# Optimization experiments

Measured on AMD Instinct MI355X. Metric: run time of the kernel, lower is better.

Reference implementation:

```python
import jax, jax.numpy as jnp
import numpy as np

N_NODES = 100000
N_EDGES = 1000000
D = 64
NUM_LAYERS = 2
NUM_REL = 3
BN_EPS = 1e-5


def setup_inputs() -> dict:
    key = jax.random.key(0)
    ks = jax.random.split(key, 10)
    h = jax.random.normal(ks[0], (N_NODES, D), dtype=jnp.float32)
    norm = jax.random.uniform(ks[1], (N_EDGES,), dtype=jnp.float32)
    src = jax.random.randint(ks[2], (N_EDGES,), 0, N_NODES, dtype=jnp.int32)
    dst = jax.random.randint(ks[3], (N_EDGES,), 0, N_NODES, dtype=jnp.int32)
    rel_type = jax.random.randint(ks[4], (N_EDGES,), 0, NUM_REL, dtype=jnp.int32)
    # learned params
    bound = np.sqrt(6.0 / D)  # kaiming_uniform fan_in, relu gain sqrt(2): sqrt(6/fan_in)
    weight = jax.random.uniform(ks[5], (NUM_REL, D, D), minval=-bound, maxval=bound, dtype=jnp.float32)
    s = 1.0 / np.sqrt(D)
    w_ih = jax.random.uniform(ks[6], (3 * D, D), minval=-s, maxval=s, dtype=jnp.float32)
    w_hh = jax.random.uniform(ks[7], (3 * D, D), minval=-s, maxval=s, dtype=jnp.float32)
    b_ih = jax.random.uniform(ks[8], (3 * D,), minval=-s, maxval=s, dtype=jnp.float32)
    b_hh = jax.random.uniform(ks[9], (3 * D,), minval=-s, maxval=s, dtype=jnp.float32)
    gamma = jnp.ones((D,), dtype=jnp.float32)
    beta = jnp.zeros((D,), dtype=jnp.float32)
    return {"h": h, "norm": norm, "weight": weight, "w_ih": w_ih, "w_hh": w_hh,
            "b_ih": b_ih, "b_hh": b_hh, "gamma": gamma, "beta": beta,
            "src": src, "dst": dst, "rel_type": rel_type}


def _gru_cell(x, h, w_ih, w_hh, b_ih, b_hh):
    # torch nn.GRU single-step math
    gi = x @ w_ih.T + b_ih  # [N, 3D]
    gh = h @ w_hh.T + b_hh
    i_r, i_z, i_n = jnp.split(gi, 3, axis=-1)
    h_r, h_z, h_n = jnp.split(gh, 3, axis=-1)
    r = jax.nn.sigmoid(i_r + h_r)
    z = jax.nn.sigmoid(i_z + h_z)
    n = jnp.tanh(i_n + r * h_n)
    return (1.0 - z) * n + z * h


def reference(h, norm, weight, w_ih, w_hh, b_ih, b_hh, gamma, beta, src, dst, rel_type):
    output = h
    hstate = jnp.zeros_like(h)
    for _ in range(NUM_LAYERS):
        # transform all node features by each relation weight, then gather per edge
        t = jnp.einsum('nd,rde->rne', output, weight)        # [R, N, D]
        msg = t[rel_type, src] * norm[:, None]               # [E, D]
        swh = jax.ops.segment_sum(msg, dst, num_segments=N_NODES)  # scatter-sum to dst
        hstate = _gru_cell(swh, hstate, w_ih, w_hh, b_ih, b_hh)
        output = hstate  # seq_len==1 GRU: output == new hidden state
    # BatchNorm1d (training mode, biased variance)
    mean = jnp.mean(output, axis=0)
    var = jnp.mean(jnp.square(output - mean), axis=0)
    return (output - mean) / jnp.sqrt(var + BN_EPS) * gamma + beta
```

## Files before the change

kernel.cpp:

```cpp
#include <hip/hip_runtime.h>

typedef __bf16 bf16x8 __attribute__((ext_vector_type(8)));
typedef float f32x4 __attribute__((ext_vector_type(4)));
typedef short short8 __attribute__((ext_vector_type(8)));

#define MFMA16(a, b, c) __builtin_amdgcn_mfma_f32_16x16x32_bf16(a, b, c, 0, 0, 0)

__device__ inline unsigned short bf16_rne(float x) {
  unsigned u = __builtin_bit_cast(unsigned, x);
  return (unsigned short)((u + 0x7FFFu + ((u >> 16) & 1u)) >> 16);
}
__device__ inline float bf16_tof(unsigned short s) {
  unsigned u = ((unsigned)s) << 16;
  return __builtin_bit_cast(float, u);
}
__device__ inline void split2(float x, unsigned short* hi, unsigned short* lo) {
  unsigned short h = bf16_rne(x);
  *hi = h;
  *lo = bf16_rne(x - bf16_tof(h));
}
__device__ inline float fast_rcp(float x) { return __builtin_amdgcn_rcpf(x); }


__global__ __launch_bounds__(256) void wprep_kernel(
    const float* __restrict__ W, const float* __restrict__ w_ih,
    const float* __restrict__ w_hh, unsigned short* __restrict__ frags) {
  int idx = blockIdx.x * 256 + threadIdx.x;
  if (idx < 1536) {
    int lane = idx & 63;
    int ks = (idx >> 6) % 6;
    int tci = idx / (6 * 64);
    int c = tci * 16 + (lane & 15);
    size_t dbase = ((size_t)(tci * 6 + ks) * 64 + lane) * 8;
#pragma unroll
    for (int j = 0; j < 8; ++j) {
      int k = ks * 32 + ((lane >> 4) << 3) + j;
      int r = k >> 6, d = k & 63;
      float v = W[(r << 12) + (d << 6) + c];
      unsigned short h, l;
      split2(v, &h, &l);
      frags[dbase + j] = h;
      frags[12288 + dbase + j] = l;
    }
  } else if (idx < 1536 + 2 * 1536) {
    int i2 = idx - 1536;
    int set = i2 / 1536;
    int i3 = i2 % 1536;
    int lane = i3 & 63;
    int ks = (i3 >> 6) & 1;
    int tci = (i3 >> 7) % 12;
    int c = tci * 16 + (lane & 15);
    unsigned short* hi = frags + (size_t)(2 + 2 * set) * 12288;
    unsigned short* lo = hi + 12288;
    size_t dbase = ((size_t)(tci * 2 + ks) * 64 + lane) * 8;
    const float* wsrc = set ? w_hh : w_ih;
#pragma unroll
    for (int j = 0; j < 8; ++j) {
      int k = ks * 32 + ((lane >> 4) << 3) + j;
      float v = wsrc[(c << 6) + k];
      unsigned short h, l;
      split2(v, &h, &l);
      hi[dbase + j] = h;
      lo[dbase + j] = l;
    }
  }
}


__global__ __launch_bounds__(256) void count_kernel(
    const int* __restrict__ dst, unsigned* __restrict__ counts, int E) {
  int base = (blockIdx.x * 256 + threadIdx.x) * 4;
  if (base + 4 <= E) {
    int4 d = *(const int4*)(dst + base);
    atomicAdd(&counts[d.x], 1u);
    atomicAdd(&counts[d.y], 1u);
    atomicAdd(&counts[d.z], 1u);
    atomicAdd(&counts[d.w], 1u);
  } else {
    for (int k = base; k < E; ++k) atomicAdd(&counts[dst[k]], 1u);
  }
}

__global__ __launch_bounds__(1024) void scan_k1(
    const unsigned* __restrict__ counts, unsigned* __restrict__ offs,
    unsigned* __restrict__ bsums, int N) {
  __shared__ unsigned sm[1024];
  int tid = threadIdx.x;
  int i = blockIdx.x * 1024 + tid;
  unsigned v = (i < N) ? counts[i] : 0u;
  sm[tid] = v;
  __syncthreads();
  for (int ofs = 1; ofs < 1024; ofs <<= 1) {
    unsigned add = (tid >= ofs) ? sm[tid - ofs] : 0u;
    __syncthreads();
    sm[tid] += add;
    __syncthreads();
  }
  if (i < N) offs[i] = sm[tid] - v;
  if (tid == 0) bsums[blockIdx.x] = sm[1023];
}

__global__ __launch_bounds__(128) void scan_k2(
    unsigned* __restrict__ bsums, unsigned* __restrict__ offs, int M, int N) {
  __shared__ unsigned sm[128];
  int tid = threadIdx.x;
  unsigned v = (tid < M) ? bsums[tid] : 0u;
  sm[tid] = v;
  __syncthreads();
  for (int ofs = 1; ofs < 128; ofs <<= 1) {
    unsigned add = (tid >= ofs) ? sm[tid - ofs] : 0u;
    __syncthreads();
    sm[tid] += add;
    __syncthreads();
  }
  if (tid < M) bsums[tid] = sm[tid] - v;
  if (tid == 127) offs[N] = sm[127];
}

__global__ __launch_bounds__(256) void scan_k3(
    unsigned* __restrict__ offs, const unsigned* __restrict__ bsums, int N) {
  int i = blockIdx.x * 256 + threadIdx.x;
  if (i < N) offs[i] = offs[i] + bsums[i >> 10];
}

__global__ __launch_bounds__(128) void bin_init_kernel(
    const unsigned* __restrict__ offs, unsigned* __restrict__ bincur, int nbins) {
  int b = threadIdx.x;
  if (b < nbins) bincur[b] = offs[b << 10];
}

#define SCHUNK 2048
__global__ __launch_bounds__(256) void bin_scatter_kernel(
    const int* __restrict__ src, const int* __restrict__ dst,
    const int* __restrict__ rel, const float* __restrict__ norm,
    unsigned* __restrict__ bincur, uint2* __restrict__ binbuf, int E) {
  __shared__ unsigned cnt[128];
  __shared__ unsigned base[128];
  int tid = threadIdx.x;
  int start = blockIdx.x * SCHUNK;
  if (tid < 128) cnt[tid] = 0u;
  __syncthreads();
  unsigned mybin[8];
  uint2 myrec[8];
#pragma unroll
  for (int i = 0; i < 8; ++i) {
    int e = start + i * 256 + tid;
    if (e < E) {
      int d = dst[e];
      mybin[i] = (unsigned)d >> 10;
      myrec[i].x = (unsigned)src[e] | ((unsigned)rel[e] << 17) |
                   ((unsigned)(d & 1023) << 19);
      myrec[i].y = __builtin_bit_cast(unsigned, norm[e]);
      atomicAdd(&cnt[mybin[i]], 1u);
    } else {
      mybin[i] = 0xFFFFFFFFu;
    }
  }
  __syncthreads();
  if (tid < 128) {
    unsigned c = cnt[tid];
    base[tid] = c ? atomicAdd(&bincur[tid], c) : 0u;
    cnt[tid] = 0u;
  }
  __syncthreads();
#pragma unroll
  for (int i = 0; i < 8; ++i) {
    if (mybin[i] != 0xFFFFFFFFu) {
      unsigned r = atomicAdd(&cnt[mybin[i]], 1u);
      binbuf[base[mybin[i]] + r] = myrec[i];
    }
  }
}

__global__ __launch_bounds__(1024) void bin_sort_kernel(
    const uint2* __restrict__ binbuf, const unsigned* __restrict__ offs,
    uint2* __restrict__ epack, unsigned* __restrict__ rcnt, int N) {
  __shared__ unsigned cnt[3 * 1024];
  __shared__ unsigned offl[1024];
  int bin = blockIdx.x;
  int base = bin << 10;
  int tid = threadIdx.x;
  int hi = base + 1024;
  if (hi > N) hi = N;
  if (base + tid < N) offl[tid] = offs[base + tid];
  cnt[tid] = 0u;
  cnt[1024 + tid] = 0u;
  cnt[2048 + tid] = 0u;
  __syncthreads();
  unsigned start = offs[base];
  unsigned end = offs[hi];
  for (unsigned j = start + tid; j < end; j += 1024) {
    uint2 rec = binbuf[j];
    unsigned dlo = rec.x >> 19;
    unsigned r = (rec.x >> 17) & 3;
    atomicAdd(&cnt[r * 1024 + dlo], 1u);
  }
  __syncthreads();
  unsigned c0 = cnt[tid], c1 = cnt[1024 + tid];
  int n = base + tid;
  if (n < N) rcnt[n] = c0 | (c1 << 16);
  unsigned o = (n < N) ? offl[tid] : 0u;
  cnt[tid] = o;
  cnt[1024 + tid] = o + c0;
  cnt[2048 + tid] = o + c0 + c1;
  __syncthreads();
  for (unsigned j = start + tid; j < end; j += 1024) {
    uint2 rec = binbuf[j];
    unsigned dlo = rec.x >> 19;
    unsigned r = (rec.x >> 17) & 3;
    unsigned p = atomicAdd(&cnt[r * 1024 + dlo], 1u);
    epack[p] = rec;
  }
}


template <int LAYER>
__global__ __launch_bounds__(256) void layer_kernel(
    const float* __restrict__ xf, const unsigned* __restrict__ offs,
    const unsigned* __restrict__ rcnt, const uint2* __restrict__ epack,
    const unsigned short* __restrict__ wft,
    const unsigned short* __restrict__ wfi, const unsigned short* __restrict__ wfh,
    const float* __restrict__ b_ih, const float* __restrict__ b_hh,
    float* __restrict__ outf, int N) {
  __shared__ float zld[16][197];
  __shared__ float swht[16][69];
  int tid = threadIdx.x;
  int n0 = blockIdx.x << 4;

  {
    int g = tid >> 4, l16 = tid & 15;
    int n = n0 + g;
    int c4 = l16 << 2;
    float z0[4] = {}, z1[4] = {}, z2[4] = {};
    if (n < N) {
      unsigned a = offs[n], b = offs[n + 1];
      unsigned rc = rcnt[n];
      unsigned b1 = a + (rc & 0xFFFFu), b2 = b1 + (rc >> 16);
      auto run = [&](unsigned s, unsigned e, float* z) {
        unsigned j = s;
        for (; j + 2 <= e; j += 2) {
          uint2 e0 = epack[j], e1 = epack[j + 1];
          float4 v0 = *(const float4*)(xf + (((size_t)(e0.x & 0x1FFFFu)) << 6) + c4);
          float4 v1 = *(const float4*)(xf + (((size_t)(e1.x & 0x1FFFFu)) << 6) + c4);
          float nv0 = __builtin_bit_cast(float, e0.y);
          float nv1 = __builtin_bit_cast(float, e1.y);
          z[0] = fmaf(nv0, v0.x, fmaf(nv1, v1.x, z[0]));
          z[1] = fmaf(nv0, v0.y, fmaf(nv1, v1.y, z[1]));
          z[2] = fmaf(nv0, v0.z, fmaf(nv1, v1.z, z[2]));
          z[3] = fmaf(nv0, v0.w, fmaf(nv1, v1.w, z[3]));
        }
        if (j < e) {
          uint2 e0 = epack[j];
          float4 v0 = *(const float4*)(xf + (((size_t)(e0.x & 0x1FFFFu)) << 6) + c4);
          float nv0 = __builtin_bit_cast(float, e0.y);
          z[0] = fmaf(nv0, v0.x, z[0]);
          z[1] = fmaf(nv0, v0.y, z[1]);
          z[2] = fmaf(nv0, v0.z, z[2]);
          z[3] = fmaf(nv0, v0.w, z[3]);
        }
      };
      run(a, b1, z0);
      run(b1, b2, z1);
      run(b2, b, z2);
    }
#pragma unroll
    for (int i = 0; i < 4; ++i) {
      zld[g][c4 + i] = z0[i];
      zld[g][64 + c4 + i] = z1[i];
      zld[g][128 + c4 + i] = z2[i];
    }
  }
  __syncthreads();

  int lane = tid & 63, w = tid >> 6;
  int r15 = lane & 15, kq = lane >> 4;
  {
    const short8* fh = (const short8*)wft;
    const short8* fl = (const short8*)(wft + 12288);
    f32x4 acc = {0.f, 0.f, 0.f, 0.f};
#pragma unroll
    for (int ks = 0; ks < 6; ++ks) {
      const float* zr = &zld[r15][ks * 32 + (kq << 3)];
      short8 th, tl;
#pragma unroll
      for (int jj = 0; jj < 8; ++jj) {
        unsigned short h_, l_;
        split2(zr[jj], &h_, &l_);
        th[jj] = (short)h_;
        tl[jj] = (short)l_;
      }
      bf16x8 ahi = __builtin_bit_cast(bf16x8, th);
      bf16x8 alo = __builtin_bit_cast(bf16x8, tl);
      bf16x8 bhi = __builtin_bit_cast(bf16x8, fh[(w * 6 + ks) * 64 + lane]);
      bf16x8 blo = __builtin_bit_cast(bf16x8, fl[(w * 6 + ks) * 64 + lane]);
      acc = MFMA16(ahi, bhi, acc);
      acc = MFMA16(ahi, blo, acc);
      acc = MFMA16(alo, bhi, acc);
    }
    int c = (w << 4) + r15;
#pragma unroll
    for (int reg = 0; reg < 4; ++reg) swht[(kq << 2) + reg][c] = acc[reg];
  }
  __syncthreads();

  {
    int c = (w << 4) + r15;
    int row = n0 + r15;
    if (row >= N) row = N - 1;

    bf16x8 axh[2], axl[2], ahh2[2], ahl2[2];
#pragma unroll
    for (int ks = 0; ks < 2; ++ks) {
      const float* sr = &swht[r15][ks * 32 + (kq << 3)];
      short8 th, tl;
#pragma unroll
      for (int jj = 0; jj < 8; ++jj) {
        unsigned short h_, l_;
        split2(sr[jj], &h_, &l_);
        th[jj] = (short)h_;
        tl[jj] = (short)l_;
      }
      axh[ks] = __builtin_bit_cast(bf16x8, th);
      axl[ks] = __builtin_bit_cast(bf16x8, tl);
    }
    if (LAYER) {
#pragma unroll
      for (int ks = 0; ks < 2; ++ks) {
        const float* hr = xf + (((size_t)row) << 6) + ks * 32 + (kq << 3);
        float4 h0 = *(const float4*)hr;
        float4 h1v = *(const float4*)(hr + 4);
        float hv[8] = {h0.x, h0.y, h0.z, h0.w, h1v.x, h1v.y, h1v.z, h1v.w};
        short8 th, tl;
#pragma unroll
        for (int jj = 0; jj < 8; ++jj) {
          unsigned short h_, l_;
          split2(hv[jj], &h_, &l_);
          th[jj] = (short)h_;
          tl[jj] = (short)l_;
        }
        ahh2[ks] = __builtin_bit_cast(bf16x8, th);
        ahl2[ks] = __builtin_bit_cast(bf16x8, tl);
      }
    }

    const short8* fih = (const short8*)wfi;
    const short8* fil = (const short8*)(wfi + 12288);
    const short8* fhh = (const short8*)wfh;
    const short8* fhl = (const short8*)(wfh + 12288);
    f32x4 accx[3], acch[3];
#pragma unroll
    for (int g = 0; g < 3; ++g) {
      accx[g] = (f32x4){0.f, 0.f, 0.f, 0.f};
      acch[g] = (f32x4){0.f, 0.f, 0.f, 0.f};
#pragma unroll
      for (int ks = 0; ks < 2; ++ks) {
        int tci = (g << 2) + w;
        bf16x8 bih = __builtin_bit_cast(bf16x8, fih[(tci * 2 + ks) * 64 + lane]);
        bf16x8 bil = __builtin_bit_cast(bf16x8, fil[(tci * 2 + ks) * 64 + lane]);
        accx[g] = MFMA16(axh[ks], bih, accx[g]);
        accx[g] = MFMA16(axh[ks], bil, accx[g]);
        accx[g] = MFMA16(axl[ks], bih, accx[g]);
        if (LAYER) {
          bf16x8 bhh = __builtin_bit_cast(bf16x8, fhh[(tci * 2 + ks) * 64 + lane]);
          bf16x8 bhl = __builtin_bit_cast(bf16x8, fhl[(tci * 2 + ks) * 64 + lane]);
          acch[g] = MFMA16(ahh2[ks], bhh, acch[g]);
          acch[g] = MFMA16(ahh2[ks], bhl, acch[g]);
          acch[g] = MFMA16(ahl2[ks], bhh, acch[g]);
        }
      }
    }

    float bi0 = b_ih[c], bi1 = b_ih[64 + c], bi2 = b_ih[128 + c];
    float bh0 = b_hh[c], bh1 = b_hh[64 + c], bh2 = b_hh[128 + c];
#pragma unroll
    for (int reg = 0; reg < 4; ++reg) {
      int n = n0 + (kq << 2) + reg;
      if (n >= N) break;
      size_t idx = (((size_t)n) << 6) + c;
      float hp = LAYER ? xf[idx] : 0.f;
      float gir = accx[0][reg] + bi0;
      float giz = accx[1][reg] + bi1;
      float gin = accx[2][reg] + bi2;
      float ghr = (LAYER ? acch[0][reg] : 0.f) + bh0;
      float ghz = (LAYER ? acch[1][reg] : 0.f) + bh1;
      float ghn = (LAYER ? acch[2][reg] : 0.f) + bh2;
      float r = fast_rcp(1.f + __expf(-(gir + ghr)));
      float z = fast_rcp(1.f + __expf(-(giz + ghz)));
      float nn = 1.f - 2.f * fast_rcp(1.f + __expf(2.f * (gin + r * ghn)));
      outf[idx] = (1.f - z) * nn + z * hp;
    }
  }
}


__global__ __launch_bounds__(256) void bn_stats_kernel(
    const float* __restrict__ h, float* __restrict__ stats, int N) {
  int tid = threadIdx.x;
  int c = tid & 63;
  float s = 0.f, ss = 0.f;
  for (int n = blockIdx.x * 4 + (tid >> 6); n < N; n += gridDim.x * 4) {
    float v = h[(size_t)n * 64 + c];
    s += v;
    ss += v * v;
  }
  __shared__ float sm[2][256];
  sm[0][tid] = s;
  sm[1][tid] = ss;
  __syncthreads();
  if (tid < 64) {
    s = sm[0][tid] + sm[0][tid + 64] + sm[0][tid + 128] + sm[0][tid + 192];
    ss = sm[1][tid] + sm[1][tid + 64] + sm[1][tid + 128] + sm[1][tid + 192];
    atomicAdd(&stats[tid], s);
    atomicAdd(&stats[64 + tid], ss);
  }
}

__global__ __launch_bounds__(256) void bn_apply_kernel(
    float* out, const float* __restrict__ stats,
    const float* __restrict__ gamma, const float* __restrict__ beta,
    int N, int total) {
  int idx = blockIdx.x * 256 + threadIdx.x;
  if (idx >= total) return;
  int c = idx & 63;
  float invN = 1.f / (float)N;
  float mean = stats[c] * invN;
  float var = stats[64 + c] * invN - mean * mean;
  float sc = rsqrtf(var + 1e-5f) * gamma[c];
  float sh = beta[c] - mean * sc;
  out[idx] = out[idx] * sc + sh;
}


extern "C" void kernel_launch(void* const* d_in, const int* in_sizes, int n_in,
                              void* d_out, int out_size, void* d_ws, size_t ws_size,
                              hipStream_t stream) {
  const float* h     = (const float*)d_in[0];
  const float* norm  = (const float*)d_in[1];
  const float* W     = (const float*)d_in[2];
  const float* w_ih  = (const float*)d_in[3];
  const float* w_hh  = (const float*)d_in[4];
  const float* b_ih  = (const float*)d_in[5];
  const float* b_hh  = (const float*)d_in[6];
  const float* gamma = (const float*)d_in[7];
  const float* beta  = (const float*)d_in[8];
  const int* src     = (const int*)d_in[9];
  const int* dst     = (const int*)d_in[10];
  const int* rel     = (const int*)d_in[11];
  float* out = (float*)d_out;

  const int N = in_sizes[0] / 64;
  const int E = in_sizes[1];
  const int NT = (N + 15) / 16;
  const int NBINS = (N + 1023) / 1024;

  char* wsp = (char*)d_ws;
  float* hf = (float*)wsp;                      wsp += (size_t)N * 64 * 4;
  unsigned short* frags = (unsigned short*)wsp; wsp += 6 * 12288 * 2;
  unsigned* offs = (unsigned*)wsp;   wsp += ((size_t)N + 4) * 4;
  unsigned* cursor = (unsigned*)wsp; wsp += (size_t)N * 4;
  unsigned* rcnt = (unsigned*)wsp;   wsp += (size_t)N * 4;
  uint2* epack = (uint2*)wsp;        wsp += (size_t)E * 8;
  unsigned* bsums = (unsigned*)wsp;  wsp += 128 * 4;
  float* stats = (float*)wsp;        wsp += 128 * 4;

  uint2* binbuf = (uint2*)hf;
  unsigned* bincur = cursor;

  const unsigned short* frag_t = frags;
  const unsigned short* frag_i = frags + 2 * 12288;
  const unsigned short* frag_h = frags + 4 * 12288;

  const int M = (N + 1023) / 1024;

  hipMemsetAsync(cursor, 0, (size_t)N * 4, stream);
  hipMemsetAsync(stats, 0, 128 * 4, stream);

  wprep_kernel<<<18, 256, 0, stream>>>(W, w_ih, w_hh, frags);

  count_kernel<<<(E / 4 + 255) / 256, 256, 0, stream>>>(dst, cursor, E);
  scan_k1<<<M, 1024, 0, stream>>>(cursor, offs, bsums, N);
  scan_k2<<<1, 128, 0, stream>>>(bsums, offs, M, N);
  scan_k3<<<(N + 255) / 256, 256, 0, stream>>>(offs, bsums, N);
  bin_init_kernel<<<1, 128, 0, stream>>>(offs, bincur, NBINS);
  bin_scatter_kernel<<<(E + SCHUNK - 1) / SCHUNK, 256, 0, stream>>>(
      src, dst, rel, norm, bincur, binbuf, E);
  bin_sort_kernel<<<NBINS, 1024, 0, stream>>>(binbuf, offs, epack, rcnt, N);

  layer_kernel<0><<<NT, 256, 0, stream>>>(h, offs, rcnt, epack, frag_t,
                                          frag_i, frag_h, b_ih, b_hh, hf, N);
  layer_kernel<1><<<NT, 256, 0, stream>>>(hf, offs, rcnt, epack, frag_t,
                                          frag_i, frag_h, b_ih, b_hh, out, N);

  bn_stats_kernel<<<256, 256, 0, stream>>>(out, stats, N);
  int total = N * 64;
  bn_apply_kernel<<<(total + 255) / 256, 256, 0, stream>>>(out, stats, gamma,
                                                           beta, N, total);
}
```

Before: 307.8 us.

## Aggregate edges per 16-node tile via LDS atomics; fuse BN stats into layer

The bin sort now does a single pass per destination, with no split by relation and no per-relation counts. The layer kernel stages chunks of the tile's edge range into shared memory, and all 256 threads spread those edges evenly, accumulating with LDS float atomics into per-node, per-relation slots. This is meant to remove load imbalance from skewed per-node degrees and drop the extra sort pass and the rcnt array. BatchNorm statistics are now reduced inside the second layer kernel, so the separate stats kernel is gone. The cost is many shared-memory atomics and non-deterministic float summation order.

```diff
diff --git a/kernel.cpp b/kernel.cpp
--- a/kernel.cpp
+++ b/kernel.cpp
@@ -174,8 +174,8 @@
 
 __global__ __launch_bounds__(1024) void bin_sort_kernel(
     const uint2* __restrict__ binbuf, const unsigned* __restrict__ offs,
-    uint2* __restrict__ epack, unsigned* __restrict__ rcnt, int N) {
-  __shared__ unsigned cnt[3 * 1024];
+    uint2* __restrict__ epack, int N) {
+  __shared__ unsigned cnt[1024];
   __shared__ unsigned offl[1024];
   int bin = blockIdx.x;
   int base = bin << 10;
@@ -184,93 +184,80 @@
   if (hi > N) hi = N;
   if (base + tid < N) offl[tid] = offs[base + tid];
   cnt[tid] = 0u;
-  cnt[1024 + tid] = 0u;
-  cnt[2048 + tid] = 0u;
   __syncthreads();
   unsigned start = offs[base];
   unsigned end = offs[hi];
   for (unsigned j = start + tid; j < end; j += 1024) {
     uint2 rec = binbuf[j];
     unsigned dlo = rec.x >> 19;
-    unsigned r = (rec.x >> 17) & 3;
-    atomicAdd(&cnt[r * 1024 + dlo], 1u);
-  }
-  __syncthreads();
-  unsigned c0 = cnt[tid], c1 = cnt[1024 + tid];
-  int n = base + tid;
-  if (n < N) rcnt[n] = c0 | (c1 << 16);
-  unsigned o = (n < N) ? offl[tid] : 0u;
-  cnt[tid] = o;
-  cnt[1024 + tid] = o + c0;
-  cnt[2048 + tid] = o + c0 + c1;
-  __syncthreads();
-  for (unsigned j = start + tid; j < end; j += 1024) {
-    uint2 rec = binbuf[j];
-    unsigned dlo = rec.x >> 19;
-    unsigned r = (rec.x >> 17) & 3;
-    unsigned p = atomicAdd(&cnt[r * 1024 + dlo], 1u);
-    epack[p] = rec;
-  }
-}
-
+    unsigned r = atomicAdd(&cnt[dlo], 1u);
+    epack[offl[dlo] + r] = rec;
+  }
+}
+
+
+#define ECH 512
 
 template <int LAYER>
 __global__ __launch_bounds__(256) void layer_kernel(
     const float* __restrict__ xf, const unsigned* __restrict__ offs,
-    const unsigned* __restrict__ rcnt, const uint2* __restrict__ epack,
-    const unsigned short* __restrict__ wft,
+    const uint2* __restrict__ epack, const unsigned short* __restrict__ wft,
     const unsigned short* __restrict__ wfi, const unsigned short* __restrict__ wfh,
     const float* __restrict__ b_ih, const float* __restrict__ b_hh,
-    float* __restrict__ outf, int N) {
-  __shared__ float zld[16][197];
-  __shared__ float swht[16][69];
+    float* __restrict__ outf, float* __restrict__ stats, int N) {
+  __shared__ float zld[16][3][66];
+  __shared__ float sbuf[16][69];
+  uint2* eld = (uint2*)&sbuf[0][0];
   int tid = threadIdx.x;
   int n0 = blockIdx.x << 4;
 
   {
-    int g = tid >> 4, l16 = tid & 15;
-    int n = n0 + g;
-    int c4 = l16 << 2;
-    float z0[4] = {}, z1[4] = {}, z2[4] = {};
-    if (n < N) {
-      unsigned a = offs[n], b = offs[n + 1];
-      unsigned rc = rcnt[n];
-      unsigned b1 = a + (rc & 0xFFFFu), b2 = b1 + (rc >> 16);
-      auto run = [&](unsigned s, unsigned e, float* z) {
-        unsigned j = s;
-        for (; j + 2 <= e; j += 2) {
-          uint2 e0 = epack[j], e1 = epack[j + 1];
-          float4 v0 = *(const float4*)(xf + (((size_t)(e0.x & 0x1FFFFu)) << 6) + c4);
-          float4 v1 = *(const float4*)(xf + (((size_t)(e1.x & 0x1FFFFu)) << 6) + c4);
-          float nv0 = __builtin_bit_cast(float, e0.y);
-          float nv1 = __builtin_bit_cast(float, e1.y);
-          z[0] = fmaf(nv0, v0.x, fmaf(nv1, v1.x, z[0]));
-          z[1] = fmaf(nv0, v0.y, fmaf(nv1, v1.y, z[1]));
-          z[2] = fmaf(nv0, v0.z, fmaf(nv1, v1.z, z[2]));
-          z[3] = fmaf(nv0, v0.w, fmaf(nv1, v1.w, z[3]));
-        }
-        if (j < e) {
-          uint2 e0 = epack[j];
-          float4 v0 = *(const float4*)(xf + (((size_t)(e0.x & 0x1FFFFu)) << 6) + c4);
-          float nv0 = __builtin_bit_cast(float, e0.y);
-          z[0] = fmaf(nv0, v0.x, z[0]);
-          z[1] = fmaf(nv0, v0.y, z[1]);
-          z[2] = fmaf(nv0, v0.z, z[2]);
-          z[3] = fmaf(nv0, v0.w, z[3]);
-        }
-      };
-      run(a, b1, z0);
-      run(b1, b2, z1);
-      run(b2, b, z2);
-    }
-#pragma unroll
-    for (int i = 0; i < 4; ++i) {
-      zld[g][c4 + i] = z0[i];
-      zld[g][64 + c4 + i] = z1[i];
-      zld[g][128 + c4 + i] = z2[i];
-    }
-  }
-  __syncthreads();
+    float* zf = &zld[0][0][0];
+    for (int i = tid; i < 16 * 3 * 66; i += 256) zf[i] = 0.f;
+  }
+  unsigned s0 = offs[n0], s1 = offs[n0 + 16];
+  unsigned n0lo = (unsigned)(n0 & 1023);
+  int q = tid & 15;
+  int c4 = q << 2;
+  unsigned eg = (unsigned)(tid >> 4);
+  __syncthreads();
+
+  for (unsigned base = s0; base < s1; base += ECH) {
+    unsigned C = s1 - base;
+    if (C > ECH) C = ECH;
+    for (unsigned j = tid; j < C; j += 256) eld[j] = epack[base + j];
+    __syncthreads();
+    unsigned e = eg;
+    for (; e + 16 < C; e += 32) {
+      uint2 r0 = eld[e];
+      uint2 r1 = eld[e + 16];
+      float4 v0 = *(const float4*)(xf + (((size_t)(r0.x & 0x1FFFFu)) << 6) + c4);
+      float4 v1 = *(const float4*)(xf + (((size_t)(r1.x & 0x1FFFFu)) << 6) + c4);
+      float nv0 = __builtin_bit_cast(float, r0.y);
+      float nv1 = __builtin_bit_cast(float, r1.y);
+      float* zp0 = &zld[(r0.x >> 19) - n0lo][(r0.x >> 17) & 3][c4];
+      float* zp1 = &zld[(r1.x >> 19) - n0lo][(r1.x >> 17) & 3][c4];
+      atomicAdd(&zp0[0], nv0 * v0.x);
+      atomicAdd(&zp0[1], nv0 * v0.y);
+      atomicAdd(&zp0[2], nv0 * v0.z);
+      atomicAdd(&zp0[3], nv0 * v0.w);
+      atomicAdd(&zp1[0], nv1 * v1.x);
+      atomicAdd(&zp1[1], nv1 * v1.y);
+      atomicAdd(&zp1[2], nv1 * v1.z);
+      atomicAdd(&zp1[3], nv1 * v1.w);
+    }
+    if (e < C) {
+      uint2 r0 = eld[e];
+      float4 v0 = *(const float4*)(xf + (((size_t)(r0.x & 0x1FFFFu)) << 6) + c4);
+      float nv0 = __builtin_bit_cast(float, r0.y);
+      float* zp0 = &zld[(r0.x >> 19) - n0lo][(r0.x >> 17) & 3][c4];
+      atomicAdd(&zp0[0], nv0 * v0.x);
+      atomicAdd(&zp0[1], nv0 * v0.y);
+      atomicAdd(&zp0[2], nv0 * v0.z);
+      atomicAdd(&zp0[3], nv0 * v0.w);
+    }
+    __syncthreads();
+  }
 
   int lane = tid & 63, w = tid >> 6;
   int r15 = lane & 15, kq = lane >> 4;
@@ -280,7 +267,7 @@
     f32x4 acc = {0.f, 0.f, 0.f, 0.f};
 #pragma unroll
     for (int ks = 0; ks < 6; ++ks) {
-      const float* zr = &zld[r15][ks * 32 + (kq << 3)];
+      const float* zr = &zld[r15][ks >> 1][((ks & 1) << 5) + (kq << 3)];
       short8 th, tl;
 #pragma unroll
       for (int jj = 0; jj < 8; ++jj) {
@@ -297,9 +284,10 @@
       acc = MFMA16(ahi, blo, acc);
       acc = MFMA16(alo, bhi, acc);
     }
+    __syncthreads();
     int c = (w << 4) + r15;
 #pragma unroll
-    for (int reg = 0; reg < 4; ++reg) swht[(kq << 2) + reg][c] = acc[reg];
+    for (int reg = 0; reg < 4; ++reg) sbuf[(kq << 2) + reg][c] = acc[reg];
   }
   __syncthreads();
 
@@ -311,7 +299,7 @@
     bf16x8 axh[2], axl[2], ahh2[2], ahl2[2];
 #pragma unroll
     for (int ks = 0; ks < 2; ++ks) {
-      const float* sr = &swht[r15][ks * 32 + (kq << 3)];
+      const float* sr = &sbuf[r15][(ks << 5) + (kq << 3)];
       short8 th, tl;
 #pragma unroll
       for (int jj = 0; jj < 8; ++jj) {
@@ -326,7 +314,7 @@
     if (LAYER) {
 #pragma unroll
       for (int ks = 0; ks < 2; ++ks) {
-        const float* hr = xf + (((size_t)row) << 6) + ks * 32 + (kq << 3);
+        const float* hr = xf + (((size_t)row) << 6) + (ks << 5) + (kq << 3);
         float4 h0 = *(const float4*)hr;
         float4 h1v = *(const float4*)(hr + 4);
         float hv[8] = {h0.x, h0.y, h0.z, h0.w, h1v.x, h1v.y, h1v.z, h1v.w};
@@ -372,6 +360,7 @@
 
     float bi0 = b_ih[c], bi1 = b_ih[64 + c], bi2 = b_ih[128 + c];
     float bh0 = b_hh[c], bh1 = b_hh[64 + c], bh2 = b_hh[128 + c];
+    float bn_s = 0.f, bn_ss = 0.f;
 #pragma unroll
     for (int reg = 0; reg < 4; ++reg) {
       int n = n0 + (kq << 2) + reg;
@@ -387,33 +376,26 @@
       float r = fast_rcp(1.f + __expf(-(gir + ghr)));
       float z = fast_rcp(1.f + __expf(-(giz + ghz)));
       float nn = 1.f - 2.f * fast_rcp(1.f + __expf(2.f * (gin + r * ghn)));
-      outf[idx] = (1.f - z) * nn + z * hp;
-    }
-  }
-}
-
-
-__global__ __launch_bounds__(256) void bn_stats_kernel(
-    const float* __restrict__ h, float* __restrict__ stats, int N) {
-  int tid = threadIdx.x;
-  int c = tid & 63;
-  float s = 0.f, ss = 0.f;
-  for (int n = blockIdx.x * 4 + (tid >> 6); n < N; n += gridDim.x * 4) {
-    float v = h[(size_t)n * 64 + c];
-    s += v;
-    ss += v * v;
-  }
-  __shared__ float sm[2][256];
-  sm[0][tid] = s;
-  sm[1][tid] = ss;
-  __syncthreads();
-  if (tid < 64) {
-    s = sm[0][tid] + sm[0][tid + 64] + sm[0][tid + 128] + sm[0][tid + 192];
-    ss = sm[1][tid] + sm[1][tid + 64] + sm[1][tid + 128] + sm[1][tid + 192];
-    atomicAdd(&stats[tid], s);
-    atomicAdd(&stats[64 + tid], ss);
-  }
-}
+      float o = (1.f - z) * nn + z * hp;
+      outf[idx] = o;
+      if (LAYER) {
+        bn_s += o;
+        bn_ss += o * o;
+      }
+    }
+    if (LAYER) {
+      bn_s += __shfl_xor(bn_s, 16);
+      bn_s += __shfl_xor(bn_s, 32);
+      bn_ss += __shfl_xor(bn_ss, 16);
+      bn_ss += __shfl_xor(bn_ss, 32);
+      if (kq == 0) {
+        atomicAdd(&stats[c], bn_s);
+        atomicAdd(&stats[64 + c], bn_ss);
+      }
+    }
+  }
+}
+
 
 __global__ __launch_bounds__(256) void bn_apply_kernel(
     float* out, const float* __restrict__ stats,
@@ -458,7 +440,6 @@
   unsigned short* frags = (unsigned short*)wsp; wsp += 6 * 12288 * 2;
   unsigned* offs = (unsigned*)wsp;   wsp += ((size_t)N + 4) * 4;
   unsigned* cursor = (unsigned*)wsp; wsp += (size_t)N * 4;
-  unsigned* rcnt = (unsigned*)wsp;   wsp += (size_t)N * 4;
   uint2* epack = (uint2*)wsp;        wsp += (size_t)E * 8;
   unsigned* bsums = (unsigned*)wsp;  wsp += 128 * 4;
   float* stats = (float*)wsp;        wsp += 128 * 4;
@@ -484,14 +465,15 @@
   bin_init_kernel<<<1, 128, 0, stream>>>(offs, bincur, NBINS);
   bin_scatter_kernel<<<(E + SCHUNK - 1) / SCHUNK, 256, 0, stream>>>(
       src, dst, rel, norm, bincur, binbuf, E);
-  bin_sort_kernel<<<NBINS, 1024, 0, stream>>>(binbuf, offs, epack, rcnt, N);
-
-  layer_kernel<0><<<NT, 256, 0, stream>>>(h, offs, rcnt, epack, frag_t,
-                                          frag_i, frag_h, b_ih, b_hh, hf, N);
-  layer_kernel<1><<<NT, 256, 0, stream>>>(hf, offs, rcnt, epack, frag_t,
-                                          frag_i, frag_h, b_ih, b_hh, out, N);
-
-  bn_stats_kernel<<<256, 256, 0, stream>>>(out, stats, N);
+  bin_sort_kernel<<<NBINS, 1024, 0, stream>>>(binbuf, offs, epack, N);
+
+  layer_kernel<0><<<NT, 256, 0, stream>>>(h, offs, epack, frag_t,
+                                          frag_i, frag_h, b_ih, b_hh,
+                                          hf, nullptr, N);
+  layer_kernel<1><<<NT, 256, 0, stream>>>(hf, offs, epack, frag_t,
+                                          frag_i, frag_h, b_ih, b_hh,
+                                          out, stats, N);
+
   int total = N * 64;
   bn_apply_kernel<<<(total + 255) / 256, 256, 0, stream>>>(out, stats, gamma,
                                                            beta, N, total);
```

Result: slower. 821.3 us (+166.8%).
